# Kernel optimization log

Measured on AMD Instinct MI355X. Metric: run time of the kernel, lower is better.

## Reference

```python
import jax, jax.numpy as jnp
import numpy as np

R = 8
EPS = 1e-08


def diff_x(t, r):
    # t: (B,C,H,W), running cumsum along H -> windowed sum along H
    left = t[:, :, r:2 * r + 1]
    middle = t[:, :, 2 * r + 1:] - t[:, :, :-2 * r - 1]
    right = t[:, :, -1:] - t[:, :, -2 * r - 1:-r - 1]
    return jnp.concatenate([left, middle, right], axis=2)


def diff_y(t, r):
    left = t[:, :, :, r:2 * r + 1]
    middle = t[:, :, :, 2 * r + 1:] - t[:, :, :, :-2 * r - 1]
    right = t[:, :, :, -1:] - t[:, :, :, -2 * r - 1:-r - 1]
    return jnp.concatenate([left, middle, right], axis=3)


def box_filter(x, r):
    return diff_y(diff_x(jnp.cumsum(x, axis=2), r).cumsum(axis=3), r)


def bilinear_align_corners(x, H, W):
    # x: (B,C,h,w) -> (B,C,H,W), matching F.interpolate(mode='bilinear', align_corners=True)
    h, w = x.shape[2], x.shape[3]
    ys = jnp.linspace(0.0, h - 1.0, H, dtype=x.dtype)
    xs = jnp.linspace(0.0, w - 1.0, W, dtype=x.dtype)
    y0 = jnp.clip(jnp.floor(ys).astype(jnp.int32), 0, h - 1)
    x0 = jnp.clip(jnp.floor(xs).astype(jnp.int32), 0, w - 1)
    y1 = jnp.clip(y0 + 1, 0, h - 1)
    x1 = jnp.clip(x0 + 1, 0, w - 1)
    wy = (ys - y0.astype(x.dtype))[:, None]   # (H,1)
    wx = (xs - x0.astype(x.dtype))[None, :]   # (1,W)
    v00 = x[:, :, y0[:, None], x0[None, :]]
    v01 = x[:, :, y0[:, None], x1[None, :]]
    v10 = x[:, :, y1[:, None], x0[None, :]]
    v11 = x[:, :, y1[:, None], x1[None, :]]
    top = v00 * (1 - wx) + v01 * wx
    bot = v10 * (1 - wx) + v11 * wx
    return top * (1 - wy) + bot * wy


def setup_inputs() -> dict:
    key = jax.random.key(0)
    k1, k2, k3 = jax.random.split(key, 3)
    lr_x = jax.random.uniform(k1, (4, 3, 512, 512), dtype=jnp.float32)
    lr_y = jax.random.uniform(k2, (4, 3, 512, 512), dtype=jnp.float32)
    hr_x = jax.random.uniform(k3, (4, 3, 2048, 2048), dtype=jnp.float32)
    return {"lr_x": lr_x, "lr_y": lr_y, "hr_x": hr_x}


def reference(lr_x, lr_y, hr_x):
    _, _, h_lr, w_lr = lr_x.shape
    _, _, h_hr, w_hr = hr_x.shape
    N = box_filter(jnp.ones((1, 1, h_lr, w_lr), dtype=lr_x.dtype), R)
    mean_x = box_filter(lr_x, R) / N
    mean_y = box_filter(lr_y, R) / N
    cov_xy = box_filter(lr_x * lr_y, R) / N - mean_x * mean_y
    var_x = box_filter(lr_x * lr_x, R) / N - mean_x * mean_x
    A = cov_xy / (var_x + EPS)
    b = mean_y - A * mean_x
    mean_A = bilinear_align_corners(A, h_hr, w_hr)
    mean_b = bilinear_align_corners(b, h_hr, w_hr)
    return mean_A * hr_x + mean_b
```

## Files before the change

### kernel.cpp

```cpp
#include <hip/hip_runtime.h>

#define RR 8
#define TILE 32
#define EXT (TILE + 2 * RR)

typedef float f4 __attribute__((ext_vector_type(4)));

__global__ __launch_bounds__(256) void k_ab(
    const float* __restrict__ lrx, const float* __restrict__ lry,
    float2* __restrict__ ABout, int H, int W) {
  __shared__ float sx[EXT][EXT];
  __shared__ float sy[EXT][EXT];
  __shared__ float hx[EXT][TILE];
  __shared__ float hy[EXT][TILE];
  __shared__ float hxy[EXT][TILE];
  __shared__ float hxx[EXT][TILE];

  const int bc = blockIdx.z;
  const size_t plane = (size_t)bc * H * W;
  const float* __restrict__ px = lrx + plane;
  const float* __restrict__ py = lry + plane;
  const int tx0 = blockIdx.x * TILE;
  const int ty0 = blockIdx.y * TILE;
  const int tid = threadIdx.y * 32 + threadIdx.x;

  const bool interior = (tx0 >= RR) && (ty0 >= RR) &&
                        (tx0 + TILE + RR <= W) && (ty0 + TILE + RR <= H);
  if (interior) {
    const size_t base = (size_t)(ty0 - RR) * W + (tx0 - RR);
    for (int i = tid; i < EXT * (EXT / 4); i += 256) {
      int r = i / (EXT / 4);
      int c4 = (i - r * (EXT / 4)) * 4;
      size_t o = base + (size_t)r * W + c4;
      *(float4*)&sx[r][c4] = *(const float4*)(px + o);
      *(float4*)&sy[r][c4] = *(const float4*)(py + o);
    }
  } else {
    for (int i = tid; i < EXT * EXT; i += 256) {
      int r = i / EXT, c = i % EXT;
      int gy = ty0 + r - RR, gx = tx0 + c - RR;
      float vx = 0.f, vy = 0.f;
      if (gy >= 0 && gy < H && gx >= 0 && gx < W) {
        size_t o = (size_t)gy * W + gx;
        vx = px[o];
        vy = py[o];
      }
      sx[r][c] = vx;
      sy[r][c] = vy;
    }
  }
  __syncthreads();

  for (int q = tid; q < EXT * (TILE / 4); q += 256) {
    int r = q >> 3;
    int c0 = (q & 7) * 4;
    float xv[20], yv[20];
#pragma unroll
    for (int t = 0; t < 5; ++t) {
      float4 x4 = *(const float4*)&sx[r][c0 + 4 * t];
      float4 y4 = *(const float4*)&sy[r][c0 + 4 * t];
      xv[4 * t + 0] = x4.x; xv[4 * t + 1] = x4.y; xv[4 * t + 2] = x4.z; xv[4 * t + 3] = x4.w;
      yv[4 * t + 0] = y4.x; yv[4 * t + 1] = y4.y; yv[4 * t + 2] = y4.z; yv[4 * t + 3] = y4.w;
    }
    float pv[20], qv[20];
#pragma unroll
    for (int i = 0; i < 20; ++i) { pv[i] = xv[i] * yv[i]; qv[i] = xv[i] * xv[i]; }
    float ax = 0.f, ay = 0.f, axy = 0.f, axx = 0.f;
#pragma unroll
    for (int i = 0; i < 17; ++i) { ax += xv[i]; ay += yv[i]; axy += pv[i]; axx += qv[i]; }
    float4 ox, oy, oxy, oxx;
    ox.x = ax; oy.x = ay; oxy.x = axy; oxx.x = axx;
#pragma unroll
    for (int j = 1; j < 4; ++j) {
      ax += xv[j + 16] - xv[j - 1];
      ay += yv[j + 16] - yv[j - 1];
      axy += pv[j + 16] - pv[j - 1];
      axx += qv[j + 16] - qv[j - 1];
      (&ox.x)[j] = ax; (&oy.x)[j] = ay; (&oxy.x)[j] = axy; (&oxx.x)[j] = axx;
    }
    *(float4*)&hx[r][c0] = ox;
    *(float4*)&hy[r][c0] = oy;
    *(float4*)&hxy[r][c0] = oxy;
    *(float4*)&hxx[r][c0] = oxx;
  }
  __syncthreads();

  const int c = threadIdx.x;
  const int r0 = threadIdx.y * 4;
  float vx[20], vy[20], vxy[20], vxx[20];
#pragma unroll
  for (int i = 0; i < 20; ++i) {
    vx[i] = hx[r0 + i][c];
    vy[i] = hy[r0 + i][c];
    vxy[i] = hxy[r0 + i][c];
    vxx[i] = hxx[r0 + i][c];
  }
  float sX = 0.f, sY = 0.f, sXY = 0.f, sXX = 0.f;
#pragma unroll
  for (int i = 0; i < 17; ++i) { sX += vx[i]; sY += vy[i]; sXY += vxy[i]; sXX += vxx[i]; }

  const int gx = tx0 + c;
  const int nx = min(gx + RR, W - 1) - max(gx - RR, 0) + 1;
#pragma unroll
  for (int j = 0; j < 4; ++j) {
    if (j > 0) {
      sX += vx[j + 16] - vx[j - 1];
      sY += vy[j + 16] - vy[j - 1];
      sXY += vxy[j + 16] - vxy[j - 1];
      sXX += vxx[j + 16] - vxx[j - 1];
    }
    const int gy = ty0 + r0 + j;
    const int ny = min(gy + RR, H - 1) - max(gy - RR, 0) + 1;
    float inv = 1.f / (float)(nx * ny);
    float mx = sX * inv;
    float my = sY * inv;
    float cov = sXY * inv - mx * my;
    float var = sXX * inv - mx * mx;
    float a = cov / (var + 1e-8f);
    float bv = my - a * mx;
    size_t o = plane + (size_t)gy * W + gx;
    ABout[o] = make_float2(a, bv);
  }
}

#define ROWS 4
__global__ __launch_bounds__(256) void k_out(
    const float2* __restrict__ AB, const float* __restrict__ hr,
    float* __restrict__ out, int hl, int wl, int Hh, int Wh) {
  const int yb = blockIdx.y * ROWS;
  const int bc = blockIdx.z;
  const int xb = blockIdx.x * 1024;
  const int tid = threadIdx.x;

  const float scy = (float)(hl - 1) / (float)(Hh - 1);
  const float scx = (float)(wl - 1) / (float)(Wh - 1);

  int v = (int)((float)yb * scy);
  if (v > hl - 1) v = hl - 1;

  const int xg = xb + tid * 4;
  float wxv[4];
  int dsel[4];
  int x00;
  {
    float fx0 = (float)xg * scx;
    x00 = (int)fx0;
    wxv[0] = fx0 - (float)x00;
    dsel[0] = 0;
#pragma unroll
    for (int j = 1; j < 4; ++j) {
      float fx = (float)(xg + j) * scx;
      int x0 = (int)fx;
      wxv[j] = fx - (float)x0;
      dsel[j] = x0 - x00;
    }
  }

  const size_t lrBase = (size_t)bc * hl * wl;
  const int xc0 = x00;
  const int xc1 = (x00 + 1 > wl - 1) ? wl - 1 : x00 + 1;
  const int xc2 = (x00 + 2 > wl - 1) ? wl - 1 : x00 + 2;
  float2 q[3][3];
#pragma unroll
  for (int rr = 0; rr < 3; ++rr) {
    int yr = v + rr;
    if (yr > hl - 1) yr = hl - 1;
    const float2* __restrict__ Rp = AB + lrBase + (size_t)yr * wl;
    q[rr][0] = Rp[xc0];
    q[rr][1] = Rp[xc1];
    q[rr][2] = Rp[xc2];
  }

  const size_t hrBase = ((size_t)bc * Hh + yb) * Wh + xg;
  f4 h[ROWS];
#pragma unroll
  for (int r = 0; r < ROWS; ++r)
    h[r] = __builtin_nontemporal_load((const f4*)(hr + hrBase + (size_t)r * Wh));

#pragma unroll
  for (int r = 0; r < ROWS; ++r) {
    float fy = (float)(yb + r) * scy;
    int y0 = (int)fy;
    if (y0 > hl - 1) y0 = hl - 1;
    int y1 = y0 + 1;
    if (y1 > hl - 1) y1 = hl - 1;
    const float wy = fy - (float)y0;
    const int i0 = y0 - v;
    const int i1 = y1 - v;
    float2 p00 = i0 ? q[1][0] : q[0][0];
    float2 p01 = i0 ? q[1][1] : q[0][1];
    float2 p02 = i0 ? q[1][2] : q[0][2];
    float2 p10 = (i1 == 0) ? q[0][0] : ((i1 == 1) ? q[1][0] : q[2][0]);
    float2 p11 = (i1 == 0) ? q[0][1] : ((i1 == 1) ? q[1][1] : q[2][1]);
    float2 p12 = (i1 == 0) ? q[0][2] : ((i1 == 1) ? q[1][2] : q[2][2]);
    float w0a = p00.x + (p10.x - p00.x) * wy;
    float w0b = p00.y + (p10.y - p00.y) * wy;
    float w1a = p01.x + (p11.x - p01.x) * wy;
    float w1b = p01.y + (p11.y - p01.y) * wy;
    float w2a = p02.x + (p12.x - p02.x) * wy;
    float w2b = p02.y + (p12.y - p02.y) * wy;
    f4 res;
#pragma unroll
    for (int j = 0; j < 4; ++j) {
      float loa = dsel[j] ? w1a : w0a;
      float lob = dsel[j] ? w1b : w0b;
      float hia = dsel[j] ? w2a : w1a;
      float hib = dsel[j] ? w2b : w1b;
      float w = wxv[j];
      float a = loa + (hia - loa) * w;
      float b = lob + (hib - lob) * w;
      res[j] = a * h[r][j] + b;
    }
    __builtin_nontemporal_store(res, (f4*)(out + hrBase + (size_t)r * Wh));
  }
}

extern "C" void kernel_launch(void* const* d_in, const int* in_sizes, int n_in,
                              void* d_out, int out_size, void* d_ws, size_t ws_size,
                              hipStream_t stream) {
  const float* lrx = (const float*)d_in[0];
  const float* lry = (const float*)d_in[1];
  const float* hrx = (const float*)d_in[2];
  float* out = (float*)d_out;

  const int BC = 12;
  const int hl = 512, wl = 512;
  const int Hh = 2048, Wh = 2048;

  float2* AB = (float2*)d_ws;

  dim3 g1(wl / TILE, hl / TILE, BC);
  dim3 b1(32, 8);
  k_ab<<<g1, b1, 0, stream>>>(lrx, lry, AB, hl, wl);

  dim3 g2(Wh / 1024, Hh / ROWS, BC);
  dim3 b2(256);
  k_out<<<g2, b2, 0, stream>>>(AB, hrx, out, hl, wl, Hh, Wh);
}
```

Measured before the change: 356.4 us.

## Make output kernel persistent with double-buffered software-pipelined loads

Replaces the 12288-block output grid with 1024 persistent blocks that each walk 12 work items. Loads for the next item (high-res rows and low-res A/b neighbours) are issued before the current item is computed, keeping more memory requests in flight per wave. The cost is higher register pressure from holding two windows, which may lower occupancy, and fewer blocks to hide latency.

```diff
diff --git a/kernel.cpp b/kernel.cpp
--- a/kernel.cpp
+++ b/kernel.cpp
@@ -124,75 +124,84 @@
 }
 
 #define ROWS 4
-__global__ __launch_bounds__(256) void k_out(
-    const float2* __restrict__ AB, const float* __restrict__ hr,
-    float* __restrict__ out, int hl, int wl, int Hh, int Wh) {
-  const int yb = blockIdx.y * ROWS;
-  const int bc = blockIdx.z;
-  const int xb = blockIdx.x * 1024;
-  const int tid = threadIdx.x;
-
-  const float scy = (float)(hl - 1) / (float)(Hh - 1);
-  const float scx = (float)(wl - 1) / (float)(Wh - 1);
-
+#define KO_BLOCKS 1024
+#define KO_ITERS 12
+
+struct KoWin {
+  float2 q[3][3];
+  f4 h[ROWS];
+  size_t hrBase;
+  int xg, v, yb;
+};
+
+__device__ __forceinline__ void ko_load(
+    int id, int tid, const float2* __restrict__ AB,
+    const float* __restrict__ hr, int hl, int wl, int Hh, int Wh,
+    float scy, float scx, KoWin& w) {
+  const int xbi = id & 1;
+  const int yg = (id >> 1) & 511;
+  const int bc = id >> 10;
+  const int yb = yg * ROWS;
+  const int xg = xbi * 1024 + tid * 4;
   int v = (int)((float)yb * scy);
   if (v > hl - 1) v = hl - 1;
-
-  const int xg = xb + tid * 4;
-  float wxv[4];
-  int dsel[4];
-  int x00;
-  {
-    float fx0 = (float)xg * scx;
-    x00 = (int)fx0;
-    wxv[0] = fx0 - (float)x00;
-    dsel[0] = 0;
-#pragma unroll
-    for (int j = 1; j < 4; ++j) {
-      float fx = (float)(xg + j) * scx;
-      int x0 = (int)fx;
-      wxv[j] = fx - (float)x0;
-      dsel[j] = x0 - x00;
-    }
-  }
-
-  const size_t lrBase = (size_t)bc * hl * wl;
-  const int xc0 = x00;
+  w.yb = yb;
+  w.xg = xg;
+  w.v = v;
+
+  const int x00 = (int)((float)xg * scx);
   const int xc1 = (x00 + 1 > wl - 1) ? wl - 1 : x00 + 1;
   const int xc2 = (x00 + 2 > wl - 1) ? wl - 1 : x00 + 2;
-  float2 q[3][3];
+  const size_t lrBase = (size_t)bc * hl * wl;
 #pragma unroll
   for (int rr = 0; rr < 3; ++rr) {
     int yr = v + rr;
     if (yr > hl - 1) yr = hl - 1;
     const float2* __restrict__ Rp = AB + lrBase + (size_t)yr * wl;
-    q[rr][0] = Rp[xc0];
-    q[rr][1] = Rp[xc1];
-    q[rr][2] = Rp[xc2];
-  }
-
-  const size_t hrBase = ((size_t)bc * Hh + yb) * Wh + xg;
-  f4 h[ROWS];
+    w.q[rr][0] = Rp[x00];
+    w.q[rr][1] = Rp[xc1];
+    w.q[rr][2] = Rp[xc2];
+  }
+
+  w.hrBase = ((size_t)bc * Hh + yb) * Wh + xg;
 #pragma unroll
   for (int r = 0; r < ROWS; ++r)
-    h[r] = __builtin_nontemporal_load((const f4*)(hr + hrBase + (size_t)r * Wh));
+    w.h[r] = __builtin_nontemporal_load((const f4*)(hr + w.hrBase + (size_t)r * Wh));
+}
+
+__device__ __forceinline__ void ko_compute(
+    const KoWin& w, float* __restrict__ out, int hl, int Wh,
+    float scy, float scx) {
+  float wxv[4];
+  int dsel[4];
+  const float fx0 = (float)w.xg * scx;
+  const int x00 = (int)fx0;
+  wxv[0] = fx0 - (float)x00;
+  dsel[0] = 0;
+#pragma unroll
+  for (int j = 1; j < 4; ++j) {
+    float fx = (float)(w.xg + j) * scx;
+    int x0 = (int)fx;
+    wxv[j] = fx - (float)x0;
+    dsel[j] = x0 - x00;
+  }
 
 #pragma unroll
   for (int r = 0; r < ROWS; ++r) {
-    float fy = (float)(yb + r) * scy;
+    float fy = (float)(w.yb + r) * scy;
     int y0 = (int)fy;
     if (y0 > hl - 1) y0 = hl - 1;
     int y1 = y0 + 1;
     if (y1 > hl - 1) y1 = hl - 1;
     const float wy = fy - (float)y0;
-    const int i0 = y0 - v;
-    const int i1 = y1 - v;
-    float2 p00 = i0 ? q[1][0] : q[0][0];
-    float2 p01 = i0 ? q[1][1] : q[0][1];
-    float2 p02 = i0 ? q[1][2] : q[0][2];
-    float2 p10 = (i1 == 0) ? q[0][0] : ((i1 == 1) ? q[1][0] : q[2][0]);
-    float2 p11 = (i1 == 0) ? q[0][1] : ((i1 == 1) ? q[1][1] : q[2][1]);
-    float2 p12 = (i1 == 0) ? q[0][2] : ((i1 == 1) ? q[1][2] : q[2][2]);
+    const int i0 = y0 - w.v;
+    const int i1 = y1 - w.v;
+    float2 p00 = i0 ? w.q[1][0] : w.q[0][0];
+    float2 p01 = i0 ? w.q[1][1] : w.q[0][1];
+    float2 p02 = i0 ? w.q[1][2] : w.q[0][2];
+    float2 p10 = (i1 == 0) ? w.q[0][0] : ((i1 == 1) ? w.q[1][0] : w.q[2][0]);
+    float2 p11 = (i1 == 0) ? w.q[0][1] : ((i1 == 1) ? w.q[1][1] : w.q[2][1]);
+    float2 p12 = (i1 == 0) ? w.q[0][2] : ((i1 == 1) ? w.q[1][2] : w.q[2][2]);
     float w0a = p00.x + (p10.x - p00.x) * wy;
     float w0b = p00.y + (p10.y - p00.y) * wy;
     float w1a = p01.x + (p11.x - p01.x) * wy;
@@ -206,12 +215,33 @@
       float lob = dsel[j] ? w1b : w0b;
       float hia = dsel[j] ? w2a : w1a;
       float hib = dsel[j] ? w2b : w1b;
-      float w = wxv[j];
-      float a = loa + (hia - loa) * w;
-      float b = lob + (hib - lob) * w;
-      res[j] = a * h[r][j] + b;
-    }
-    __builtin_nontemporal_store(res, (f4*)(out + hrBase + (size_t)r * Wh));
+      float wxj = wxv[j];
+      float a = loa + (hia - loa) * wxj;
+      float b = lob + (hib - lob) * wxj;
+      res[j] = a * w.h[r][j] + b;
+    }
+    __builtin_nontemporal_store(res, (f4*)(out + w.hrBase + (size_t)r * Wh));
+  }
+}
+
+__global__ __launch_bounds__(256) void k_out(
+    const float2* __restrict__ AB, const float* __restrict__ hr,
+    float* __restrict__ out, int hl, int wl, int Hh, int Wh) {
+  const int tid = threadIdx.x;
+  const float scy = (float)(hl - 1) / (float)(Hh - 1);
+  const float scx = (float)(wl - 1) / (float)(Wh - 1);
+
+  KoWin w0, w1;
+  int id = blockIdx.x;
+  ko_load(id, tid, AB, hr, hl, wl, Hh, Wh, scy, scx, w0);
+#pragma unroll 1
+  for (int k = 0; k < KO_ITERS; k += 2) {
+    ko_load(id + KO_BLOCKS, tid, AB, hr, hl, wl, Hh, Wh, scy, scx, w1);
+    ko_compute(w0, out, hl, Wh, scy, scx);
+    if (k + 2 < KO_ITERS)
+      ko_load(id + 2 * KO_BLOCKS, tid, AB, hr, hl, wl, Hh, Wh, scy, scx, w0);
+    ko_compute(w1, out, hl, Wh, scy, scx);
+    id += 2 * KO_BLOCKS;
   }
 }
 
@@ -233,7 +263,7 @@
   dim3 b1(32, 8);
   k_ab<<<g1, b1, 0, stream>>>(lrx, lry, AB, hl, wl);
 
-  dim3 g2(Wh / 1024, Hh / ROWS, BC);
+  dim3 g2(KO_BLOCKS);
   dim3 b2(256);
   k_out<<<g2, b2, 0, stream>>>(AB, hrx, out, hl, wl, Hh, Wh);
 }
```

New measurement: 360.5 us. Within noise of the previous version (+1.2%).
